# Optimization experiments

Hardware: AMD Instinct MI355X
Metric: run time of the kernel (lower is better)

Reference implementation:

```python
import jax, jax.numpy as jnp
import numpy as np

E = 1024
H = 16
DH = E // H
FF = 4 * E
EPS = 1e-5


def _layer_norm(x, g, b):
    mu = jnp.mean(x, axis=-1, keepdims=True)
    var = jnp.var(x, axis=-1, keepdims=True)
    return (x - mu) * jax.lax.rsqrt(var + EPS) * g + b


def setup_inputs() -> dict:
    key = jax.random.key(0)
    ks = jax.random.split(key, 12)
    B, S = 2, 2048
    s_e = 1.0 / np.sqrt(E)
    s_f = 1.0 / np.sqrt(FF)
    return {
        "hidden_states": jax.random.normal(ks[0], (B, S, E), jnp.float32),
        "attention_mask": jnp.zeros((B, S), jnp.float32),
        "position_bias": jax.random.normal(ks[1], (H, S, S), jnp.float32) * 0.1,
        "Wq": jax.random.normal(ks[2], (E, E), jnp.float32) * s_e,
        "bq": jnp.zeros((E,), jnp.float32),
        "Wk": jax.random.normal(ks[3], (E, E), jnp.float32) * s_e,
        "bk": jnp.zeros((E,), jnp.float32),
        "Wv": jax.random.normal(ks[4], (E, E), jnp.float32) * s_e,
        "bv": jnp.zeros((E,), jnp.float32),
        "Wo": jax.random.normal(ks[5], (E, E), jnp.float32) * s_e,
        "bo": jnp.zeros((E,), jnp.float32),
        "ln1_g": jnp.ones((E,), jnp.float32),
        "ln1_b": jnp.zeros((E,), jnp.float32),
        "W1": jax.random.normal(ks[6], (E, FF), jnp.float32) * s_e,
        "b1": jnp.zeros((FF,), jnp.float32),
        "W2": jax.random.normal(ks[7], (FF, E), jnp.float32) * s_f,
        "b2": jnp.zeros((E,), jnp.float32),
        "ln2_g": jnp.ones((E,), jnp.float32),
        "ln2_b": jnp.zeros((E,), jnp.float32),
    }


def reference(hidden_states, attention_mask, position_bias, Wq, bq, Wk, bk, Wv, bv,
              Wo, bo, ln1_g, ln1_b, W1, b1, W2, b2, ln2_g, ln2_b):
    B, S, _ = hidden_states.shape
    x = hidden_states
    # QKV projections, split heads: [B, S, H, DH]
    q = (x @ Wq + bq).reshape(B, S, H, DH)
    k = (x @ Wk + bk).reshape(B, S, H, DH)
    v = (x @ Wv + bv).reshape(B, S, H, DH)
    # scores: [B, H, S, S]
    scores = jnp.einsum("bshd,bthd->bhst", q, k) / np.sqrt(DH).astype(np.float32)
    scores = scores + position_bias[None] + attention_mask[:, None, None, :]
    probs = jax.nn.softmax(scores, axis=-1)  # dropout is identity in eval
    ctx = jnp.einsum("bhst,bthd->bshd", probs, v).reshape(B, S, E)
    attn_out = ctx @ Wo + bo
    h = _layer_norm(x + attn_out, ln1_g, ln1_b)
    ffn = jax.nn.gelu(h @ W1 + b1, approximate=False) @ W2 + b2
    return _layer_norm(h + ffn, ln2_g, ln2_b)
```

## Files before the change

kernel.cpp:

```cpp
#include <hip/hip_runtime.h>
#include <stdint.h>

#define EDIM   1024
#define NHEAD  16
#define DHEAD  64
#define FFDIM  4096
#define SEQLEN 2048
#define NBATCH 2
#define MROWS  (NBATCH * SEQLEN)
#define NT     (SEQLEN / 64)

typedef __attribute__((ext_vector_type(8))) short bf16x8;
typedef __attribute__((ext_vector_type(4))) float f32x4;

static __device__ __forceinline__ unsigned short f2bf(float f) {
    union { float f; uint32_t u; } v; v.f = f;
    return (unsigned short)((v.u + 0x7fffu + ((v.u >> 16) & 1u)) >> 16);
}

static __device__ __forceinline__ void gload16(const void* g, void* s) {
    __builtin_amdgcn_global_load_lds(
        (const __attribute__((address_space(1))) unsigned int*)g,
        (__attribute__((address_space(3))) unsigned int*)s,
        16, 0, 0);
}

__global__ void k_cast_bf16(const float* __restrict__ in, unsigned short* __restrict__ out, int n4) {
    int i = blockIdx.x * blockDim.x + threadIdx.x;
    if (i < n4) {
        float4 v = ((const float4*)in)[i];
        ushort4 o;
        o.x = f2bf(v.x); o.y = f2bf(v.y); o.z = f2bf(v.z); o.w = f2bf(v.w);
        ((ushort4*)out)[i] = o;
    }
}

__global__ void k_transpose_cast(const float* __restrict__ in, unsigned short* __restrict__ out,
                                 int R, int C) {
    __shared__ float tile[32][33];
    int c0 = blockIdx.x * 32, r0 = blockIdx.y * 32;
    int tx = threadIdx.x, ty = threadIdx.y;
    #pragma unroll
    for (int i = 0; i < 32; i += 8)
        tile[ty + i][tx] = in[(size_t)(r0 + ty + i) * C + c0 + tx];
    __syncthreads();
    #pragma unroll
    for (int i = 0; i < 32; i += 8)
        out[(size_t)(c0 + ty + i) * R + r0 + tx] = f2bf(tile[tx][ty + i]);
}

__global__ void k_transpose_v(const unsigned short* __restrict__ V, int vstride,
                              unsigned short* __restrict__ Vt) {
    __shared__ unsigned short tile[32][33];
    const int bh = blockIdx.z, b = bh >> 4, h = bh & 15;
    const int s0 = blockIdx.x * 32, d0 = blockIdx.y * 32;
    const int tx = threadIdx.x, ty = threadIdx.y;
    #pragma unroll
    for (int i = 0; i < 32; i += 8)
        tile[ty + i][tx] = V[(size_t)(b * SEQLEN + s0 + ty + i) * vstride + h * DHEAD + d0 + tx];
    __syncthreads();
    #pragma unroll
    for (int i = 0; i < 32; i += 8)
        Vt[((size_t)(b * NHEAD + h) * DHEAD + d0 + ty + i) * SEQLEN + s0 + tx] = tile[tx][ty + i];
}

__global__ void k_concat_bias(const float* __restrict__ bq, const float* __restrict__ bk,
                              const float* __restrict__ bv, float* __restrict__ out) {
    int i = blockIdx.x * 256 + threadIdx.x;
    const float* src = (i < 1024) ? bq : (i < 2048) ? bk : bv;
    out[i] = src[i & 1023];
}

template <int TBM, int TBN, int EPI>
__global__ __launch_bounds__(256, 2) void k_gemm(
    const unsigned short* __restrict__ A,
    const unsigned short* __restrict__ Bt,
    const float* __restrict__ bias,
    void* __restrict__ Cout, int M, int N, int K)
{
    constexpr int MR = TBM / 32, NR = TBN / 32;
    __shared__ __attribute__((aligned(16))) unsigned short Asm[TBM * 64];
    __shared__ __attribute__((aligned(16))) unsigned short Bsm[TBN * 64];

    const int nbx = gridDim.x;
    const int flat = blockIdx.y * nbx + blockIdx.x;
    const int cpx = (nbx * gridDim.y) >> 3;
    const int swz = (flat & 7) * cpx + (flat >> 3);
    const int bx = swz % nbx, by = swz / nbx;

    const int row0 = by * TBM, col0 = bx * TBN;
    const int t = threadIdx.x;
    const int lane = t & 63, w = t >> 6;
    const int wm = w >> 1, wn = w & 1;
    const int l15 = lane & 15, l4 = lane >> 4;
    const int sr = lane >> 3, sc = (lane & 7) * 8;

    f32x4 acc[MR][NR];
    #pragma unroll
    for (int m = 0; m < MR; ++m)
        #pragma unroll
        for (int n = 0; n < NR; ++n) acc[m][n] = (f32x4){0.f, 0.f, 0.f, 0.f};

    for (int k0 = 0; k0 < K; k0 += 64) {
        #pragma unroll
        for (int i = 0; i < TBM / 32; ++i) {
            const int r = w * (TBM / 4) + i * 8;
            gload16(A + (size_t)(row0 + r + sr) * K + k0 + sc, &Asm[r * 64]);
        }
        #pragma unroll
        for (int i = 0; i < TBN / 32; ++i) {
            const int r = w * (TBN / 4) + i * 8;
            gload16(Bt + (size_t)(col0 + r + sr) * K + k0 + sc, &Bsm[r * 64]);
        }
        __syncthreads();
        #pragma unroll
        for (int kk = 0; kk < 64; kk += 32) {
            bf16x8 af[MR], bf[NR];
            #pragma unroll
            for (int m = 0; m < MR; ++m)
                af[m] = *(const bf16x8*)&Asm[(wm * (TBM / 2) + m * 16 + l15) * 64 + kk + l4 * 8];
            #pragma unroll
            for (int n = 0; n < NR; ++n)
                bf[n] = *(const bf16x8*)&Bsm[(wn * (TBN / 2) + n * 16 + l15) * 64 + kk + l4 * 8];
            #pragma unroll
            for (int m = 0; m < MR; ++m)
                #pragma unroll
                for (int n = 0; n < NR; ++n)
                    acc[m][n] = __builtin_amdgcn_mfma_f32_16x16x32_bf16(af[m], bf[n], acc[m][n], 0, 0, 0);
        }
        __syncthreads();
    }

    #pragma unroll
    for (int m = 0; m < MR; ++m) {
        int rb = row0 + wm * (TBM / 2) + m * 16 + l4 * 4;
        #pragma unroll
        for (int n = 0; n < NR; ++n) {
            int c = col0 + wn * (TBN / 2) + n * 16 + l15;
            float bv = bias[c];
            #pragma unroll
            for (int i = 0; i < 4; ++i) {
                float v = acc[m][n][i] + bv;
                if (EPI == 1) v = 0.5f * v * (1.0f + erff(v * 0.70710678118654752f));
                if (EPI == 2) ((float*)Cout)[(size_t)(rb + i) * N + c] = v;
                else          ((unsigned short*)Cout)[(size_t)(rb + i) * N + c] = f2bf(v);
            }
        }
    }
}

__global__ __launch_bounds__(512, 2) void k_attn(
    const unsigned short* __restrict__ QKV,
    const unsigned short* __restrict__ Vt,
    const float* __restrict__ pbias,
    const float* __restrict__ mask,
    unsigned short* __restrict__ Ctx)
{
    __shared__ __attribute__((aligned(16))) unsigned short Ksm[2][64 * 72];
    __shared__ __attribute__((aligned(16))) unsigned short Vsm[2][64 * 72];
    __shared__ __attribute__((aligned(16))) unsigned short Psm[8][16 * 72];

    const int flat = blockIdx.x;
    const int swz = (flat & 7) * 64 + (flat >> 3);
    const int qt = swz & 31;
    const int h  = swz >> 5;

    const int t = threadIdx.x;
    const int lane = t & 63, w = t >> 6;
    const int wb = w & 1;
    const int wq = (w >> 1) * 16;
    const int l15 = lane & 15, l4 = lane >> 4;
    const int qrow = qt * 64 + wq;

    const float* pbrow = pbias + ((size_t)h * SEQLEN + qrow + l4 * 4) * SEQLEN;
    const float* mrow  = mask + wb * SEQLEN;

    bf16x8 qf0, qf1;
    {
        const unsigned short* qp = QKV + (size_t)(wb * SEQLEN + qrow + l15) * (3 * EDIM) + h * DHEAD + l4 * 8;
        bf16x8 r0 = *(const bf16x8*)qp;
        bf16x8 r1 = *(const bf16x8*)(qp + 32);
        #pragma unroll
        for (int e = 0; e < 8; ++e) {
            union { uint32_t u; float f; } c0, c1;
            c0.u = (uint32_t)(unsigned short)r0[e] << 16;
            c1.u = (uint32_t)(unsigned short)r1[e] << 16;
            r0[e] = (short)f2bf(c0.f * 0.125f);
            r1[e] = (short)f2bf(c1.f * 0.125f);
        }
        qf0 = r0; qf1 = r1;
    }

    f32x4 oacc[4];
    #pragma unroll
    for (int nd = 0; nd < 4; ++nd) oacc[nd] = (f32x4){0.f, 0.f, 0.f, 0.f};
    float m_run[4] = {-1e30f, -1e30f, -1e30f, -1e30f};
    float l_run[4] = {0.f, 0.f, 0.f, 0.f};

    for (int kt = 0; kt < NT; ++kt) {
        #pragma unroll
        for (int j = 0; j < 4; ++j) {
            int cid = j * 512 + t;
            int tile = cid >> 9;
            int r = (cid >> 3) & 63;
            int c = (cid & 7) * 8;
            int bb = tile & 1;
            if (tile < 2)
                *(float4*)&Ksm[bb][r * 72 + c] =
                    *(const float4*)(QKV + (size_t)(bb * SEQLEN + kt * 64 + r) * (3 * EDIM) + EDIM + h * DHEAD + c);
            else
                *(float4*)&Vsm[bb][r * 72 + c] =
                    *(const float4*)(Vt + ((size_t)((bb * NHEAD + h) * DHEAD + r)) * SEQLEN + kt * 64 + c);
        }
        __syncthreads();

        float p[4][4];
        float tmax[4] = {-1e30f, -1e30f, -1e30f, -1e30f};
        #pragma unroll
        for (int n = 0; n < 4; ++n) {
            const int scol = kt * 64 + n * 16 + l15;
            const float mk = mrow[scol];
            f32x4 z;
            #pragma unroll
            for (int i = 0; i < 4; ++i) z[i] = pbrow[(size_t)i * SEQLEN + scol] + mk;
            bf16x8 kb0 = *(const bf16x8*)&Ksm[wb][(n * 16 + l15) * 72 + l4 * 8];
            bf16x8 kb1 = *(const bf16x8*)&Ksm[wb][(n * 16 + l15) * 72 + 32 + l4 * 8];
            z = __builtin_amdgcn_mfma_f32_16x16x32_bf16(qf0, kb0, z, 0, 0, 0);
            z = __builtin_amdgcn_mfma_f32_16x16x32_bf16(qf1, kb1, z, 0, 0, 0);
            #pragma unroll
            for (int i = 0; i < 4; ++i) {
                p[n][i] = z[i];
                tmax[i] = fmaxf(tmax[i], z[i]);
            }
        }
        #pragma unroll
        for (int i = 0; i < 4; ++i) {
            float mv = tmax[i];
            #pragma unroll
            for (int off = 1; off < 16; off <<= 1) mv = fmaxf(mv, __shfl_xor(mv, off, 64));
            float mnew = fmaxf(m_run[i], mv);
            float alpha = __expf(m_run[i] - mnew);
            m_run[i] = mnew;
            float sum = 0.f;
            #pragma unroll
            for (int n = 0; n < 4; ++n) { p[n][i] = __expf(p[n][i] - mnew); sum += p[n][i]; }
            #pragma unroll
            for (int off = 1; off < 16; off <<= 1) sum += __shfl_xor(sum, off, 64);
            l_run[i] = l_run[i] * alpha + sum;
            #pragma unroll
            for (int nd = 0; nd < 4; ++nd) oacc[nd][i] *= alpha;
        }
        #pragma unroll
        for (int n = 0; n < 4; ++n)
            #pragma unroll
            for (int i = 0; i < 4; ++i)
                Psm[w][(l4 * 4 + i) * 72 + n * 16 + l15] = f2bf(p[n][i]);
        #pragma unroll
        for (int kk = 0; kk < 2; ++kk) {
            bf16x8 pa = *(const bf16x8*)&Psm[w][l15 * 72 + kk * 32 + l4 * 8];
            #pragma unroll
            for (int nd = 0; nd < 4; ++nd) {
                bf16x8 vf = *(const bf16x8*)&Vsm[wb][(nd * 16 + l15) * 72 + kk * 32 + l4 * 8];
                oacc[nd] = __builtin_amdgcn_mfma_f32_16x16x32_bf16(pa, vf, oacc[nd], 0, 0, 0);
            }
        }
        __syncthreads();
    }

    #pragma unroll
    for (int nd = 0; nd < 4; ++nd)
        #pragma unroll
        for (int i = 0; i < 4; ++i) {
            float v = oacc[nd][i] / l_run[i];
            Ctx[(size_t)(wb * SEQLEN + qrow + l4 * 4 + i) * EDIM + h * DHEAD + nd * 16 + l15] = f2bf(v);
        }
}

template <int WRITE_BF>
__global__ __launch_bounds__(256) void k_ln(
    const float* __restrict__ X, const float* __restrict__ T,
    const float* __restrict__ gam, const float* __restrict__ bet,
    float* __restrict__ Of, unsigned short* __restrict__ Ob)
{
    const int r = blockIdx.x;
    const int t = threadIdx.x;
    const size_t base = (size_t)r * EDIM + t * 4;
    float4 xv = *(const float4*)(X + base);
    float4 tv = *(const float4*)(T + base);
    float4 s = make_float4(xv.x + tv.x, xv.y + tv.y, xv.z + tv.z, xv.w + tv.w);
    float sum = s.x + s.y + s.z + s.w;
    float sq  = s.x * s.x + s.y * s.y + s.z * s.z + s.w * s.w;
    #pragma unroll
    for (int off = 1; off < 64; off <<= 1) {
        sum += __shfl_xor(sum, off, 64);
        sq  += __shfl_xor(sq,  off, 64);
    }
    __shared__ float red[8];
    const int lane = t & 63, w = t >> 6;
    if (lane == 0) { red[w] = sum; red[4 + w] = sq; }
    __syncthreads();
    sum = red[0] + red[1] + red[2] + red[3];
    sq  = red[4] + red[5] + red[6] + red[7];
    const float mu = sum * (1.0f / EDIM);
    const float var = sq * (1.0f / EDIM) - mu * mu;
    const float rs = rsqrtf(var + 1e-5f);
    float4 gv = *(const float4*)(gam + t * 4);
    float4 bv = *(const float4*)(bet + t * 4);
    float4 o = make_float4((s.x - mu) * rs * gv.x + bv.x,
                           (s.y - mu) * rs * gv.y + bv.y,
                           (s.z - mu) * rs * gv.z + bv.z,
                           (s.w - mu) * rs * gv.w + bv.w);
    *(float4*)(Of + base) = o;
    if (WRITE_BF) {
        ushort4 ob;
        ob.x = f2bf(o.x); ob.y = f2bf(o.y); ob.z = f2bf(o.z); ob.w = f2bf(o.w);
        *(ushort4*)(Ob + base) = ob;
    }
}

extern "C" void kernel_launch(void* const* d_in, const int* in_sizes, int n_in,
                              void* d_out, int out_size, void* d_ws, size_t ws_size,
                              hipStream_t stream) {
    const float* x    = (const float*)d_in[0];
    const float* mask = (const float*)d_in[1];
    const float* pb   = (const float*)d_in[2];
    const float* Wq = (const float*)d_in[3];  const float* bq = (const float*)d_in[4];
    const float* Wk = (const float*)d_in[5];  const float* bk = (const float*)d_in[6];
    const float* Wv = (const float*)d_in[7];  const float* bv = (const float*)d_in[8];
    const float* Wo = (const float*)d_in[9];  const float* bo = (const float*)d_in[10];
    const float* g1 = (const float*)d_in[11]; const float* be1 = (const float*)d_in[12];
    const float* W1 = (const float*)d_in[13]; const float* b1 = (const float*)d_in[14];
    const float* W2 = (const float*)d_in[15]; const float* b2 = (const float*)d_in[16];
    const float* g2 = (const float*)d_in[17]; const float* be2 = (const float*)d_in[18];
    float* out = (float*)d_out;

    char* ws = (char*)d_ws;
    const size_t MB = 1024 * 1024;
    unsigned short* qkv  = (unsigned short*)(ws + 0);
    unsigned short* gbf  = (unsigned short*)(ws + 0);
    unsigned short* xb   = (unsigned short*)(ws + 24 * MB);
    unsigned short* vt   = (unsigned short*)(ws + 24 * MB);
    unsigned short* wqt  = (unsigned short*)(ws + 32 * MB);
    unsigned short* wkt  = (unsigned short*)(ws + 34 * MB);
    unsigned short* wvt  = (unsigned short*)(ws + 36 * MB);
    unsigned short* wot  = (unsigned short*)(ws + 38 * MB);
    unsigned short* w1t  = (unsigned short*)(ws + 40 * MB);
    unsigned short* w2t  = (unsigned short*)(ws + 48 * MB);
    float*          bcat = (float*)(ws + 56 * MB);
    unsigned short* ctxb = (unsigned short*)(ws + 56 * MB);
    float*          t1   = (float*)(ws + 64 * MB);
    float*          hf   = (float*)(ws + 80 * MB);
    unsigned short* hb   = (unsigned short*)(ws + 96 * MB);

    const dim3 b256(256);
    const dim3 tb(32, 8);

    k_cast_bf16<<<dim3(MROWS * EDIM / 4 / 256), b256, 0, stream>>>(x, xb, MROWS * EDIM / 4);
    k_transpose_cast<<<dim3(EDIM / 32, EDIM / 32), tb, 0, stream>>>(Wq, wqt, EDIM, EDIM);
    k_transpose_cast<<<dim3(EDIM / 32, EDIM / 32), tb, 0, stream>>>(Wk, wkt, EDIM, EDIM);
    k_transpose_cast<<<dim3(EDIM / 32, EDIM / 32), tb, 0, stream>>>(Wv, wvt, EDIM, EDIM);
    k_transpose_cast<<<dim3(EDIM / 32, EDIM / 32), tb, 0, stream>>>(Wo, wot, EDIM, EDIM);
    k_transpose_cast<<<dim3(FFDIM / 32, EDIM / 32), tb, 0, stream>>>(W1, w1t, EDIM, FFDIM);
    k_transpose_cast<<<dim3(EDIM / 32, FFDIM / 32), tb, 0, stream>>>(W2, w2t, FFDIM, EDIM);
    k_concat_bias<<<dim3(12), b256, 0, stream>>>(bq, bk, bv, bcat);

    k_gemm<128, 128, 0><<<dim3(3 * EDIM / 128, MROWS / 128), b256, 0, stream>>>(
        xb, wqt, bcat, qkv, MROWS, 3 * EDIM, EDIM);
    k_transpose_v<<<dim3(SEQLEN / 32, DHEAD / 32, NBATCH * NHEAD), tb, 0, stream>>>(
        qkv + 2 * EDIM, 3 * EDIM, vt);

    k_attn<<<dim3(512), dim3(512), 0, stream>>>(qkv, vt, pb, mask, ctxb);

    k_gemm<128, 64, 2><<<dim3(EDIM / 64, MROWS / 128), b256, 0, stream>>>(
        ctxb, wot, bo, t1, MROWS, EDIM, EDIM);
    k_ln<1><<<dim3(MROWS), b256, 0, stream>>>(x, t1, g1, be1, hf, hb);
    k_gemm<128, 128, 1><<<dim3(FFDIM / 128, MROWS / 128), b256, 0, stream>>>(
        hb, w1t, b1, gbf, MROWS, FFDIM, EDIM);
    k_gemm<128, 64, 2><<<dim3(EDIM / 64, MROWS / 128), b256, 0, stream>>>(
        gbf, w2t, b2, t1, MROWS, EDIM, FFDIM);
    k_ln<0><<<dim3(MROWS), b256, 0, stream>>>(hf, t1, g2, be2, out, nullptr);
    (void)in_sizes; (void)n_in; (void)out_size; (void)ws_size;
}
```

Baseline: 408.5 us.

## Double-buffer K/V tiles with async global-to-LDS loads and XOR swizzle

```diff
diff --git a/kernel.cpp b/kernel.cpp
--- a/kernel.cpp
+++ b/kernel.cpp
@@ -156,9 +156,9 @@
     const float* __restrict__ mask,
     unsigned short* __restrict__ Ctx)
 {
-    __shared__ __attribute__((aligned(16))) unsigned short Ksm[2][64 * 72];
-    __shared__ __attribute__((aligned(16))) unsigned short Vsm[2][64 * 72];
-    __shared__ __attribute__((aligned(16))) unsigned short Psm[8][16 * 72];
+    __shared__ __attribute__((aligned(16))) unsigned short Ksm[2][2][64 * 64];
+    __shared__ __attribute__((aligned(16))) unsigned short Vsm[2][2][64 * 64];
+    __shared__ __attribute__((aligned(16))) unsigned short Psm[8][16 * 64];
 
     const int flat = blockIdx.x;
     const int swz = (flat & 7) * 64 + (flat >> 3);
@@ -197,34 +197,42 @@
     float m_run[4] = {-1e30f, -1e30f, -1e30f, -1e30f};
     float l_run[4] = {0.f, 0.f, 0.f, 0.f};
 
-    for (int kt = 0; kt < NT; ++kt) {
+    const int srow = lane >> 3;
+    const int schk = lane & 7;
+
+    auto stage = [&](int buf, int kt) {
+        const int kbase = kt * 64;
         #pragma unroll
         for (int j = 0; j < 4; ++j) {
-            int cid = j * 512 + t;
-            int tile = cid >> 9;
-            int r = (cid >> 3) & 63;
-            int c = (cid & 7) * 8;
-            int bb = tile & 1;
-            if (tile < 2)
-                *(float4*)&Ksm[bb][r * 72 + c] =
-                    *(const float4*)(QKV + (size_t)(bb * SEQLEN + kt * 64 + r) * (3 * EDIM) + EDIM + h * DHEAD + c);
+            const int q  = w * 4 + j;
+            const int kv = q >> 4;
+            const int bb = (q >> 3) & 1;
+            const int g  = q & 7;
+            const int row = g * 8 + srow;
+            const int cg  = (schk ^ (row & 7)) * 8;
+            if (kv == 0)
+                gload16(QKV + (size_t)(bb * SEQLEN + kbase + row) * (3 * EDIM) + EDIM + h * DHEAD + cg,
+                        &Ksm[buf][bb][g * 512]);
             else
-                *(float4*)&Vsm[bb][r * 72 + c] =
-                    *(const float4*)(Vt + ((size_t)((bb * NHEAD + h) * DHEAD + r)) * SEQLEN + kt * 64 + c);
-        }
-        __syncthreads();
-
+                gload16(Vt + ((size_t)((bb * NHEAD + h) * DHEAD) + row) * SEQLEN + kbase + cg,
+                        &Vsm[buf][bb][g * 512]);
+        }
+    };
+
+    auto compute = [&](int buf, int kt) {
+        const int kbase = kt * 64;
         float p[4][4];
         float tmax[4] = {-1e30f, -1e30f, -1e30f, -1e30f};
+        const int r7 = l15 & 7;
         #pragma unroll
         for (int n = 0; n < 4; ++n) {
-            const int scol = kt * 64 + n * 16 + l15;
+            const int scol = kbase + n * 16 + l15;
             const float mk = mrow[scol];
             f32x4 z;
             #pragma unroll
             for (int i = 0; i < 4; ++i) z[i] = pbrow[(size_t)i * SEQLEN + scol] + mk;
-            bf16x8 kb0 = *(const bf16x8*)&Ksm[wb][(n * 16 + l15) * 72 + l4 * 8];
-            bf16x8 kb1 = *(const bf16x8*)&Ksm[wb][(n * 16 + l15) * 72 + 32 + l4 * 8];
+            bf16x8 kb0 = *(const bf16x8*)&Ksm[buf][wb][(n * 16 + l15) * 64 + ((l4 ^ r7) << 3)];
+            bf16x8 kb1 = *(const bf16x8*)&Ksm[buf][wb][(n * 16 + l15) * 64 + (((4 + l4) ^ r7) << 3)];
             z = __builtin_amdgcn_mfma_f32_16x16x32_bf16(qf0, kb0, z, 0, 0, 0);
             z = __builtin_amdgcn_mfma_f32_16x16x32_bf16(qf1, kb1, z, 0, 0, 0);
             #pragma unroll
@@ -253,18 +261,30 @@
         #pragma unroll
         for (int n = 0; n < 4; ++n)
             #pragma unroll
-            for (int i = 0; i < 4; ++i)
-                Psm[w][(l4 * 4 + i) * 72 + n * 16 + l15] = f2bf(p[n][i]);
+            for (int i = 0; i < 4; ++i) {
+                const int row = l4 * 4 + i;
+                const int col = n * 16 + l15;
+                Psm[w][row * 64 + (((col >> 3) ^ (row & 7)) << 3) + (col & 7)] = f2bf(p[n][i]);
+            }
         #pragma unroll
         for (int kk = 0; kk < 2; ++kk) {
-            bf16x8 pa = *(const bf16x8*)&Psm[w][l15 * 72 + kk * 32 + l4 * 8];
+            bf16x8 pa = *(const bf16x8*)&Psm[w][l15 * 64 + (((kk * 4 + l4) ^ r7) << 3)];
             #pragma unroll
             for (int nd = 0; nd < 4; ++nd) {
-                bf16x8 vf = *(const bf16x8*)&Vsm[wb][(nd * 16 + l15) * 72 + kk * 32 + l4 * 8];
+                bf16x8 vf = *(const bf16x8*)&Vsm[buf][wb][(nd * 16 + l15) * 64 + (((kk * 4 + l4) ^ r7) << 3)];
                 oacc[nd] = __builtin_amdgcn_mfma_f32_16x16x32_bf16(pa, vf, oacc[nd], 0, 0, 0);
             }
         }
+    };
+
+    stage(0, 0);
+    __syncthreads();
+    int buf = 0;
+    for (int kt = 0; kt < NT; ++kt) {
+        stage(buf ^ 1, (kt + 1) & (NT - 1));
+        compute(buf, kt);
         __syncthreads();
+        buf ^= 1;
     }
 
     #pragma unroll
```

Measured after the change: 398.1 us. -2.5%, faster.
